# Performance work log

Hardware: AMD Instinct MI355X
Metric: run time of the kernel (lower is better)

Reference implementation:

```python
import jax, jax.numpy as jnp
import numpy as np

N = 50000   # nodes
E = 800000  # edges (avg degree 16)
D = 128     # node feature dim
DE = 16     # edge feature dim
H = 128     # MLP hidden dim
MSG_IN = 2 * D + DE + 1  # src feat + dst feat + edge feat + squared distance


def setup_inputs() -> dict:
    key = jax.random.key(0)
    ks = jax.random.split(key, 10)
    def wmat(k, shp):
        return jax.random.normal(k, shp, jnp.float32) * 0.05
    return {
        "f": jax.random.normal(ks[0], (N, D), jnp.float32),
        "x": jax.random.normal(ks[1], (N, 3), jnp.float32),
        "w": jax.random.normal(ks[2], (E, DE), jnp.float32),
        "src": jax.random.randint(ks[3], (E,), 0, N),
        "dst": jax.random.randint(ks[4], (E,), 0, N),
        "Wm1": wmat(ks[5], (MSG_IN, H)), "bm1": jnp.zeros((H,), jnp.float32),
        "Wm2": wmat(ks[6], (H, D)),      "bm2": jnp.zeros((D,), jnp.float32),
        "Wu1": wmat(ks[7], (D, H)),      "bu1": jnp.zeros((H,), jnp.float32),
        "Wu2": wmat(ks[8], (H, D)),      "bu2": jnp.zeros((D,), jnp.float32),
    }


def reference(f, x, w, src, dst, Wm1, bm1, Wm2, bm2, Wu1, bu1, Wu2, bu2):
    # message: gather endpoint features, squared distance, concat, MLP  [E, D]
    sqd = jnp.sum((x[src] - x[dst]) ** 2, axis=-1, keepdims=True)  # [E, 1]
    msg_in = jnp.concatenate([f[src], f[dst], w, sqd], axis=-1)    # [E, MSG_IN]
    m = jnp.dot(jax.nn.relu(jnp.dot(msg_in, Wm1) + bm1), Wm2) + bm2  # [E, D]
    # reduce: sum messages at destination nodes (DGL fn.sum)
    m_sum = jax.ops.segment_sum(m, dst, num_segments=N)             # [N, D]
    # update: node MLP on m_sum + f
    h = m_sum + f
    f_new = jnp.dot(jax.nn.relu(jnp.dot(h, Wu1) + bu1), Wu2) + bu2  # [N, D]
    return f_new
```

## Files before the change

### kernel.cpp

```cpp
#include <hip/hip_runtime.h>
#include <hip/hip_fp8.h>

#define D 128
#define HD 128
#define DE 16
#define MSG_IN 273
#define EB 64
#define NT 256
#define KP1 288
#define NCH2 4
#define NB 32
#define HID_PAD 132
#define CH8 (4 * EB * 64)
#define LDS1 (4 * EB * 64 + EB * 32)
#define OB 8192
#define OC 24576

typedef __attribute__((ext_vector_type(8))) short short8v;
typedef __attribute__((ext_vector_type(4))) float f32x4;
typedef __attribute__((ext_vector_type(2))) float f32x2;
typedef unsigned short ushort_t;
typedef unsigned char uchar_t;

#define GLOAD_LDS16(gp, lp) \
    __builtin_amdgcn_global_load_lds((const __attribute__((address_space(1))) unsigned int*)(gp), \
                                     (__attribute__((address_space(3))) unsigned int*)(lp), 16, 0, 0)

__device__ __forceinline__ unsigned short f2bf(float v) {
    unsigned int u = __builtin_bit_cast(unsigned int, v);
    u += 0x7fffu + ((u >> 16) & 1u);
    return (unsigned short)(u >> 16);
}
__device__ __forceinline__ float bf2f(ushort_t u) {
    return __builtin_bit_cast(float, (unsigned int)u << 16);
}
__device__ __forceinline__ unsigned int cvt_pk_bf16(float lo, float hi) {
    unsigned int r;
    asm("v_cvt_pk_bf16_f32 %0, %1, %2" : "=v"(r) : "v"(lo), "v"(hi));
    return r;
}
__device__ __forceinline__ uchar_t f8e(float v) {
    __hip_fp8_e4m3 t(v);
    return (uchar_t)t.__x;
}
__device__ __forceinline__ float f8d(unsigned b) {
    unsigned t = ((b & 0x7fu) << 20) | ((b & 0x80u) << 24);
    return __builtin_bit_cast(float, t) * 0x1p120f;
}

__global__ void fused_pre_kernel(const float* __restrict__ Wm1, const float* __restrict__ Wm2,
                                 const float* __restrict__ Wu1, const float* __restrict__ Wu2,
                                 ushort_t* __restrict__ W1p, ushort_t* __restrict__ W2p,
                                 ushort_t* __restrict__ Wu1p, ushort_t* __restrict__ Wu2p,
                                 const int* __restrict__ dst, int* __restrict__ cnt,
                                 int E) {
    const int gid    = blockIdx.x * 256 + threadIdx.x;
    const int stride = gridDim.x * 256;
    const int rp1 = 128 * KP1;
    const int rp2 = rp1 + HD * D;
    const int rp_elems = rp2 + 2 * HD * D;
    for (int i = gid; i < rp_elems; i += stride) {
        if (i < rp1) {
            int n = i / KP1, k = i % KP1;
            W1p[i] = f2bf((k < MSG_IN) ? Wm1[(size_t)k * HD + n] : 0.f);
        } else if (i < rp2) {
            int i2 = i - rp1;
            int n = i2 / HD, k = i2 % HD;
            W2p[i2] = f2bf(Wm2[(size_t)k * D + n]);
        } else {
            int i2 = (i - rp2);
            const bool second = i2 >= HD * D;
            if (second) i2 -= HD * D;
            int n = i2 / HD, k = i2 % HD;
            if (second) Wu2p[i2] = f2bf(Wu2[(size_t)k * D + n]);
            else        Wu1p[i2] = f2bf(Wu1[(size_t)k * HD + n]);
        }
    }
    for (int i = gid; i < E; i += stride) atomicAdd(&cnt[dst[i]], 1);
}

__global__ __launch_bounds__(1024) void scan_kernel(const int* __restrict__ cnt,
                                                    int* __restrict__ roff,
                                                    int* __restrict__ cursor, int Nn) {
    __shared__ int wsum[16];
    const int t = threadIdx.x, l = t & 63, wid = t >> 6;
    int running = 0;
    for (int base = 0; base < Nn; base += 4096) {
        const int i0 = base + t * 4;
        int v0 = 0, v1 = 0, v2 = 0, v3 = 0;
        if (i0 + 3 < Nn) {
            int4 v = *(const int4*)(cnt + i0);
            v0 = v.x; v1 = v.y; v2 = v.z; v3 = v.w;
        } else {
            if (i0 + 0 < Nn) v0 = cnt[i0 + 0];
            if (i0 + 1 < Nn) v1 = cnt[i0 + 1];
            if (i0 + 2 < Nn) v2 = cnt[i0 + 2];
        }
        const int vsum = v0 + v1 + v2 + v3;
        int s = vsum;
        #pragma unroll
        for (int off = 1; off < 64; off <<= 1) {
            int u = __shfl_up(s, off, 64);
            if (l >= off) s += u;
        }
        if (l == 63) wsum[wid] = s;
        __syncthreads();
        if (wid == 0 && l < 16) {
            int xv = wsum[l];
            #pragma unroll
            for (int off = 1; off < 16; off <<= 1) {
                int u = __shfl_up(xv, off, 64);
                if (l >= off) xv += u;
            }
            wsum[l] = xv;
        }
        __syncthreads();
        const int prev  = (wid > 0) ? wsum[wid - 1] : 0;
        const int total = wsum[15];
        int ex = running + prev + (s - vsum);
        if (i0 + 0 < Nn) { roff[i0 + 0] = ex; cursor[i0 + 0] = ex; } ex += v0;
        if (i0 + 1 < Nn) { roff[i0 + 1] = ex; cursor[i0 + 1] = ex; } ex += v1;
        if (i0 + 2 < Nn) { roff[i0 + 2] = ex; cursor[i0 + 2] = ex; } ex += v2;
        if (i0 + 3 < Nn) { roff[i0 + 3] = ex; cursor[i0 + 3] = ex; }
        running += total;
        __syncthreads();
    }
}

__global__ __launch_bounds__(NT, 4) void mid_kernel(
    const int* __restrict__ dst, int* cursor,
    const int* __restrict__ roff, const int* __restrict__ cnt,
    int* __restrict__ perm, int* __restrict__ sdst,
    const float* __restrict__ w, ushort_t* __restrict__ wbf,
    float* __restrict__ mh,
    const float* __restrict__ f, const ushort_t* __restrict__ W1p,
    uchar_t* __restrict__ Af, ushort_t* __restrict__ Bf16,
    int E, int Nn, int SB)
{
    if ((int)blockIdx.x < SB) {
        const int gid    = blockIdx.x * 256 + threadIdx.x;
        const int stride = SB * 256;
        for (int i = gid; i < E; i += stride) {
            int d = dst[i];
            int s = atomicAdd(&cursor[d], 1);
            perm[s] = i;
            sdst[s] = d;
            const float* wp = w + (size_t)i * DE;
            ushort_t* op = wbf + (size_t)i * DE;
            #pragma unroll
            for (int q = 0; q < 2; ++q) {
                float4 v0 = *(const float4*)(wp + q * 8);
                float4 v1 = *(const float4*)(wp + q * 8 + 4);
                union { ushort_t us[8]; short8v v; } pk;
                pk.us[0] = f2bf(v0.x); pk.us[1] = f2bf(v0.y);
                pk.us[2] = f2bf(v0.z); pk.us[3] = f2bf(v0.w);
                pk.us[4] = f2bf(v1.x); pk.us[5] = f2bf(v1.y);
                pk.us[6] = f2bf(v1.z); pk.us[7] = f2bf(v1.w);
                *(short8v*)(op + q * 8) = pk.v;
            }
        }
        for (int n = gid; n < Nn; n += stride) {
            const int c = cnt[n];
            const int r = roff[n];
            const bool need0 = (c == 0) || (r / EB != (r + c - 1) / EB);
            if (need0) {
                float4 z = {0.f, 0.f, 0.f, 0.f};
                float* p = mh + (size_t)n * D;
                #pragma unroll
                for (int k = 0; k < 32; ++k) *(float4*)(p + k * 4) = z;
            }
        }
        return;
    }

    __shared__ __align__(16) ushort_t lds[2 * 64 * 64];

    const int t    = threadIdx.x;
    const int lane = t & 63;
    const int wv   = t >> 6;
    const int col  = lane & 15;
    const int g    = lane >> 4;
    const int n0   = ((int)blockIdx.x - SB) * 64;

    #pragma unroll
    for (int it = 0; it < 4; ++it) {
        const int gidx = it * 256 + t;
        const int row  = gidx >> 4;
        const int gr   = gidx & 15;
        const int pair = gr >> 3, s = gr & 7;
        const int sP   = s ^ (row & 7);
        const int gn   = min(n0 + row, Nn - 1);
        const size_t off = (size_t)gn * D + gr * 8;
        float4 v0 = *(const float4*)(f + off);
        float4 v1 = *(const float4*)(f + off + 4);
        union { ushort_t us[8]; short8v v; } pk;
        pk.us[0] = f2bf(v0.x); pk.us[1] = f2bf(v0.y);
        pk.us[2] = f2bf(v0.z); pk.us[3] = f2bf(v0.w);
        pk.us[4] = f2bf(v1.x); pk.us[5] = f2bf(v1.y);
        pk.us[6] = f2bf(v1.z); pk.us[7] = f2bf(v1.w);
        *(short8v*)&lds[(pair * 64 + row) * 64 + sP * 8] = pk.v;
    }
    __syncthreads();

    #pragma unroll
    for (int half = 0; half < 2; ++half) {
        f32x4 acc[4][2];
        #pragma unroll
        for (int rt = 0; rt < 4; ++rt) {
            acc[rt][0] = (f32x4){0.f, 0.f, 0.f, 0.f};
            acc[rt][1] = (f32x4){0.f, 0.f, 0.f, 0.f};
        }
        const int kbase = half * 128;
        #pragma unroll
        for (int c = 0; c < 4; ++c) {
            short8v b0 = *(const short8v*)&W1p[(size_t)(wv * 32 + col) * KP1 + kbase + c * 32 + g * 8];
            short8v b1 = *(const short8v*)&W1p[(size_t)(wv * 32 + 16 + col) * KP1 + kbase + c * 32 + g * 8];
            short8v a[4];
            #pragma unroll
            for (int rt = 0; rt < 4; ++rt) {
                const int row = rt * 16 + col;
                const int sP = (((c & 1) << 2) + g) ^ (row & 7);
                a[rt] = *(const short8v*)&lds[((c >> 1) * 64 + row) * 64 + sP * 8];
            }
            #pragma unroll
            for (int rt = 0; rt < 4; ++rt) {
                acc[rt][0] = __builtin_amdgcn_mfma_f32_16x16x32_bf16(a[rt], b0, acc[rt][0], 0, 0, 0);
                acc[rt][1] = __builtin_amdgcn_mfma_f32_16x16x32_bf16(a[rt], b1, acc[rt][1], 0, 0, 0);
            }
        }
        #pragma unroll
        for (int rt = 0; rt < 4; ++rt)
            #pragma unroll
            for (int r = 0; r < 4; ++r) {
                const int row = rt * 16 + g * 4 + r;
                const int gn = n0 + row;
                if (gn < Nn) {
                    const int cp = wv * 32 + col * 2;
                    if (half == 0) {
                        ushort_t pk = (ushort_t)f8e(acc[rt][0][r]) |
                                      ((ushort_t)f8e(acc[rt][1][r]) << 8);
                        *(ushort_t*)(Af + (size_t)gn * D + cp) = pk;
                    } else {
                        *(unsigned int*)(Bf16 + (size_t)gn * D + cp) =
                            cvt_pk_bf16(acc[rt][0][r], acc[rt][1][r]);
                    }
                }
            }
    }
}

__global__ __launch_bounds__(NT, 5) void edge_lin_kernel(
    const uchar_t* __restrict__ Af, const ushort_t* __restrict__ Bf16,
    const float* __restrict__ x, const ushort_t* __restrict__ wbf,
    const int* __restrict__ src,
    const int* __restrict__ perm, const int* __restrict__ sdst,
    const ushort_t* __restrict__ W1p, const float* __restrict__ bm1,
    float* __restrict__ mh, int E)
{
    __shared__ __align__(16) uchar_t lds8[28672];
    __shared__ int s_rid[EB];
    __shared__ int s_dgs[EB];

    const int t    = threadIdx.x;
    const int lane = t & 63;
    const int wv   = t >> 6;
    const int e0   = blockIdx.x * EB;
    const int nvalid = min(EB, E - e0);

    const int myd  = (e0 + lane < E) ? sdst[e0 + lane] : -1;
    const int prevd = (e0 > 0) ? sdst[e0 - 1] : -2;
    const int nextd = (e0 + EB < E) ? sdst[e0 + EB] : -2;

    const int dprev_l = __shfl_up(myd, 1, 64);
    const bool head = (lane == 0) || (myd != dprev_l);
    const unsigned long long mask = __ballot(head && (lane < nvalid));
    const unsigned long long le = (lane == 63) ? ~0ull : ((1ull << (lane + 1)) - 1ull);
    const int rid = (int)__popcll(mask & le) - 1;
    const int ndist = (int)__popcll(mask);
    s_rid[lane] = (rid < 0) ? 0 : rid;
    if (head && lane < nvalid) s_dgs[rid] = myd;

    {
        const int el8 = lane >> 3;
        const int s   = lane & 7;
        const int sl  = s ^ el8;
        const int slA = min(e0 + wv * 16 + el8,     E - 1);
        const int slB = min(e0 + wv * 16 + 8 + el8, E - 1);
        const int nsA = src[perm[slA]];
        const int nsB = src[perm[slB]];
        GLOAD_LDS16(Af + (size_t)nsA * D + sl * 16, &lds8[(wv * 16    ) * 128]);
        GLOAD_LDS16(Af + (size_t)nsB * D + sl * 16, &lds8[(wv * 16 + 8) * 128]);
    }
    {
        const int ntask = ndist * 16;
        for (int idx = t; idx < ntask; idx += NT) {
            const int rowr = idx >> 4;
            const int gr   = idx & 15;
            const int dg   = s_dgs[rowr];
            uint4 v = *(const uint4*)(Bf16 + (size_t)dg * D + gr * 8);
            const int phys = gr ^ (rowr & 15);
            *(uint4*)&lds8[OB + rowr * 256 + phys * 16] = v;
        }
    }
    {
        const int el = lane >> 2, q = lane & 3;
        const int qp = q ^ (el & 3);
        const int slot = e0 + wv * 16 + el;
        const bool ok = slot < E;
        const int sc = min(slot, E - 1);
        const int ge = perm[sc];
        union { ushort_t us[8]; short8v v; } pk;
        #pragma unroll
        for (int j = 0; j < 8; ++j) pk.us[j] = 0;
        if (ok) {
            if (q < 2) {
                pk.v = *(const short8v*)(wbf + (size_t)ge * DE + q * 8);
            } else if (q == 2) {
                const int ns = src[ge], nd = sdst[sc];
                float dx = x[ns*3+0] - x[nd*3+0];
                float dy = x[ns*3+1] - x[nd*3+1];
                float dz = x[ns*3+2] - x[nd*3+2];
                pk.us[0] = f2bf(dx*dx + dy*dy + dz*dz);
            }
        }
        *(short8v*)&lds8[OC + (wv * 16 + el) * 64 + qp * 16] = pk.v;
    }

    const int col = lane & 15;
    const int g   = lane >> 4;

    short8v bc0 = *(const short8v*)&W1p[(size_t)(wv * 32 + col) * KP1 + 256 + g * 8];
    short8v bc1 = *(const short8v*)&W1p[(size_t)(wv * 32 + 16 + col) * KP1 + 256 + g * 8];

    __syncthreads();

    f32x4 acc[4][2];
    {
        float bv0 = bm1[wv * 32 + col];
        float bv1 = bm1[wv * 32 + 16 + col];
        #pragma unroll
        for (int rt = 0; rt < 4; ++rt) {
            acc[rt][0] = (f32x4){bv0, bv0, bv0, bv0};
            acc[rt][1] = (f32x4){bv1, bv1, bv1, bv1};
        }
    }
    #pragma unroll
    for (int rt = 0; rt < 4; ++rt) {
        const int row = rt * 16 + col;
        const int sP8 = g ^ (row & 3);
        short8v a = *(const short8v*)&lds8[OC + row * 64 + sP8 * 16];
        acc[rt][0] = __builtin_amdgcn_mfma_f32_16x16x32_bf16(a, bc0, acc[rt][0], 0, 0, 0);
        acc[rt][1] = __builtin_amdgcn_mfma_f32_16x16x32_bf16(a, bc1, acc[rt][1], 0, 0, 0);
    }

    float h[4][2][4];
    const int cgA = 2 * wv + (col >> 3);
    const int coA = (col * 2) & 15;
    const int cbB = 4 * wv + (col >> 2);
    const int coB = (col & 3) * 4;
    #pragma unroll
    for (int rt = 0; rt < 4; ++rt) {
        #pragma unroll
        for (int r = 0; r < 4; ++r) {
            const int row = rt * 16 + g * 4 + r;
            const int rd  = s_rid[row];
            const int aadr = row * 128 + ((cgA ^ (row & 7)) << 4) + coA;
            const int badr = OB + rd * 256 + ((cbB ^ (rd & 15)) << 4) + coB;
            const ushort_t ap = *(const ushort_t*)&lds8[aadr];
            const unsigned bp = *(const unsigned*)&lds8[badr];
            f32x2 af = __builtin_amdgcn_cvt_pk_f32_fp8((int)ap, false);
            const float b0f = __builtin_bit_cast(float, bp << 16);
            const float b1f = __builtin_bit_cast(float, bp & 0xffff0000u);
            h[rt][0][r] = fmaxf(acc[rt][0][r] + af[0] + b0f, 0.f);
            h[rt][1][r] = fmaxf(acc[rt][1][r] + af[1] + b1f, 0.f);
        }
    }

    float qs[4][2];
    #pragma unroll
    for (int rt = 0; rt < 4; ++rt) {
        qs[rt][0] = (h[rt][0][0] + h[rt][0][1]) + (h[rt][0][2] + h[rt][0][3]);
        qs[rt][1] = (h[rt][1][0] + h[rt][1][1]) + (h[rt][1][2] + h[rt][1][3]);
    }
    unsigned long long rem = mask;
    while (rem) {
        const int beg = (int)__builtin_ctzll(rem);
        rem &= rem - 1;
        const int end = rem ? (int)__builtin_ctzll(rem) : nvalid;
        const int dg  = __shfl(myd, beg, 64);

        float s0 = 0.f, s1 = 0.f;
        #pragma unroll
        for (int rt = 0; rt < 4; ++rt) {
            const int qb = rt * 16 + g * 4;
            const int lo = max(qb, beg);
            const int hi = min(qb + 4, end);
            if (lo < hi) {
                if (lo == qb && hi == qb + 4) {
                    s0 += qs[rt][0]; s1 += qs[rt][1];
                } else {
                    #pragma unroll
                    for (int r = 0; r < 4; ++r) {
                        const int sl = qb + r;
                        if (sl >= beg && sl < end) {
                            s0 += h[rt][0][r]; s1 += h[rt][1][r];
                        }
                    }
                }
            }
        }
        s0 += __shfl_xor(s0, 16, 64); s0 += __shfl_xor(s0, 32, 64);
        s1 += __shfl_xor(s1, 16, 64); s1 += __shfl_xor(s1, 32, 64);
        if (g == 0) {
            const bool bnd = (beg == 0 && dg == prevd) || (end == nvalid && dg == nextd);
            float* p = mh + (size_t)dg * D + wv * 32 + col;
            if (bnd) { atomicAdd(p, s0); atomicAdd(p + 16, s1); }
            else     { p[0] = s0; p[16] = s1; }
        }
    }
}

__global__ __launch_bounds__(NT, 4) void node_fused_kernel(
    const float* __restrict__ f, const float* __restrict__ mh,
    const int* __restrict__ cnt,
    const ushort_t* __restrict__ W2p, const float* __restrict__ bm2,
    const ushort_t* __restrict__ Wu1p, const float* __restrict__ bu1,
    const ushort_t* __restrict__ Wu2p, const float* __restrict__ bu2,
    float* __restrict__ out, int Nn)
{
    __shared__ __align__(16) ushort_t lds[2 * 64 * 64];
    __shared__ int s_cnt[64];

    const int t    = threadIdx.x;
    const int lane = t & 63;
    const int wv   = t >> 6;
    const int col  = lane & 15;
    const int g    = lane >> 4;
    const int n0   = blockIdx.x * 64;

    if (t < 64) s_cnt[t] = (n0 + t < Nn) ? cnt[n0 + t] : 0;

    #pragma unroll
    for (int it = 0; it < 4; ++it) {
        const int gidx = it * 256 + t;
        const int row  = gidx >> 4;
        const int gr   = gidx & 15;
        const int pair = gr >> 3, s = gr & 7;
        const int sP   = s ^ (row & 7);
        const int gn   = n0 + row;
        union { ushort_t us[8]; short8v v; } pk;
        if (gn < Nn) {
            const size_t off = (size_t)gn * D + gr * 8;
            float4 m0 = *(const float4*)(mh + off);
            float4 m1 = *(const float4*)(mh + off + 4);
            pk.us[0] = f2bf(m0.x); pk.us[1] = f2bf(m0.y);
            pk.us[2] = f2bf(m0.z); pk.us[3] = f2bf(m0.w);
            pk.us[4] = f2bf(m1.x); pk.us[5] = f2bf(m1.y);
            pk.us[6] = f2bf(m1.z); pk.us[7] = f2bf(m1.w);
        } else {
            #pragma unroll
            for (int j = 0; j < 8; ++j) pk.us[j] = 0;
        }
        *(short8v*)&lds[(pair * 64 + row) * 64 + sP * 8] = pk.v;
    }
    __syncthreads();

    f32x4 acc[4][2];
    {
        const float bv0 = bm2[wv * 32 + col];
        const float bv1 = bm2[wv * 32 + 16 + col];
        #pragma unroll
        for (int rt = 0; rt < 4; ++rt)
            #pragma unroll
            for (int r = 0; r < 4; ++r) {
                const float cn = (float)s_cnt[rt * 16 + g * 4 + r];
                acc[rt][0][r] = cn * bv0;
                acc[rt][1][r] = cn * bv1;
            }
    }
    #pragma unroll
    for (int c = 0; c < 4; ++c) {
        short8v b0 = *(const short8v*)&W2p[(size_t)(wv * 32 + col) * HD + c * 32 + g * 8];
        short8v b1 = *(const short8v*)&W2p[(size_t)(wv * 32 + 16 + col) * HD + c * 32 + g * 8];
        short8v a[4];
        #pragma unroll
        for (int rt = 0; rt < 4; ++rt) {
            const int row = rt * 16 + col;
            const int sP = (((c & 1) << 2) + g) ^ (row & 7);
            a[rt] = *(const short8v*)&lds[((c >> 1) * 64 + row) * 64 + sP * 8];
        }
        #pragma unroll
        for (int rt = 0; rt < 4; ++rt) {
            acc[rt][0] = __builtin_amdgcn_mfma_f32_16x16x32_bf16(a[rt], b0, acc[rt][0], 0, 0, 0);
            acc[rt][1] = __builtin_amdgcn_mfma_f32_16x16x32_bf16(a[rt], b1, acc[rt][1], 0, 0, 0);
        }
    }
    __syncthreads();

    const int ph = wv >> 1;
    #pragma unroll
    for (int rt = 0; rt < 4; ++rt)
        #pragma unroll
        for (int r = 0; r < 4; ++r) {
            const int row = rt * 16 + g * 4 + r;
            const int gn = n0 + row;
            #pragma unroll
            for (int j = 0; j < 2; ++j) {
                const int ca = wv * 32 + j * 16 + col;
                float v = 0.f;
                if (gn < Nn) v = acc[rt][j][r] + f[(size_t)gn * D + ca];
                unsigned int pk2 = cvt_pk_bf16(v, v);
                const int sH = (((wv & 1) << 2) + j * 2 + (col >> 3)) ^ (row & 7);
                lds[(ph * 64 + row) * 64 + sH * 8 + (col & 7)] = (ushort_t)pk2;
            }
        }
    __syncthreads();

    const size_t wrow0 = (size_t)(wv * 32 + col) * HD;
    const size_t wrow1 = (size_t)(wv * 32 + 16 + col) * HD;
    f32x4 acc1[4][2];
    {
        float bv0 = bu1[wv * 32 + col];
        float bv1 = bu1[wv * 32 + 16 + col];
        #pragma unroll
        for (int rt = 0; rt < 4; ++rt) {
            acc1[rt][0] = (f32x4){bv0, bv0, bv0, bv0};
            acc1[rt][1] = (f32x4){bv1, bv1, bv1, bv1};
        }
    }
    #pragma unroll
    for (int c = 0; c < 4; ++c) {
        short8v b0 = *(const short8v*)&Wu1p[wrow0 + c * 32 + g * 8];
        short8v b1 = *(const short8v*)&Wu1p[wrow1 + c * 32 + g * 8];
        short8v a[4];
        #pragma unroll
        for (int rt = 0; rt < 4; ++rt) {
            const int row = rt * 16 + col;
            const int sP = (((c & 1) << 2) + g) ^ (row & 7);
            a[rt] = *(const short8v*)&lds[((c >> 1) * 64 + row) * 64 + sP * 8];
        }
        #pragma unroll
        for (int rt = 0; rt < 4; ++rt) {
            acc1[rt][0] = __builtin_amdgcn_mfma_f32_16x16x32_bf16(a[rt], b0, acc1[rt][0], 0, 0, 0);
            acc1[rt][1] = __builtin_amdgcn_mfma_f32_16x16x32_bf16(a[rt], b1, acc1[rt][1], 0, 0, 0);
        }
    }
    __syncthreads();

    #pragma unroll
    for (int rt = 0; rt < 4; ++rt)
        #pragma unroll
        for (int j = 0; j < 2; ++j)
            #pragma unroll
            for (int r = 0; r < 4; ++r) {
                const int row = rt * 16 + g * 4 + r;
                float v = fmaxf(acc1[rt][j][r], 0.f);
                unsigned int pk2 = cvt_pk_bf16(v, v);
                const int sH = (((wv & 1) << 2) + j * 2 + (col >> 3)) ^ (row & 7);
                lds[(ph * 64 + row) * 64 + sH * 8 + (col & 7)] = (ushort_t)pk2;
            }
    __syncthreads();

    f32x4 acc2[4][2];
    {
        float bv0 = bu2[wv * 32 + col];
        float bv1 = bu2[wv * 32 + 16 + col];
        #pragma unroll
        for (int rt = 0; rt < 4; ++rt) {
            acc2[rt][0] = (f32x4){bv0, bv0, bv0, bv0};
            acc2[rt][1] = (f32x4){bv1, bv1, bv1, bv1};
        }
    }
    #pragma unroll
    for (int c = 0; c < 4; ++c) {
        short8v b0 = *(const short8v*)&Wu2p[wrow0 + c * 32 + g * 8];
        short8v b1 = *(const short8v*)&Wu2p[wrow1 + c * 32 + g * 8];
        short8v a[4];
        #pragma unroll
        for (int rt = 0; rt < 4; ++rt) {
            const int row = rt * 16 + col;
            const int sP = (((c & 1) << 2) + g) ^ (row & 7);
            a[rt] = *(const short8v*)&lds[((c >> 1) * 64 + row) * 64 + sP * 8];
        }
        #pragma unroll
        for (int rt = 0; rt < 4; ++rt) {
            acc2[rt][0] = __builtin_amdgcn_mfma_f32_16x16x32_bf16(a[rt], b0, acc2[rt][0], 0, 0, 0);
            acc2[rt][1] = __builtin_amdgcn_mfma_f32_16x16x32_bf16(a[rt], b1, acc2[rt][1], 0, 0, 0);
        }
    }

    #pragma unroll
    for (int rt = 0; rt < 4; ++rt)
        #pragma unroll
        for (int r = 0; r < 4; ++r) {
            const int row = rt * 16 + g * 4 + r;
            const int gn = n0 + row;
            if (gn < Nn) {
                out[(size_t)gn * D + wv * 32 + col]      = acc2[rt][0][r];
                out[(size_t)gn * D + wv * 32 + 16 + col] = acc2[rt][1][r];
            }
        }
}


__global__ void repack_kernel(const float* __restrict__ Wm1, const float* __restrict__ Wm2,
                              ushort_t* __restrict__ W1p, ushort_t* __restrict__ W2p) {
    int idx = blockIdx.x * 256 + threadIdx.x;
    const int n1 = 128 * KP1;
    if (idx < n1) {
        int n = idx / KP1, k = idx % KP1;
        W1p[idx] = f2bf((k < MSG_IN) ? Wm1[(size_t)k * HD + n] : 0.f);
    } else {
        int i2 = idx - n1;
        if (i2 < HD * D) {
            int n = i2 / HD, k = i2 % HD;
            W2p[i2] = f2bf(Wm2[(size_t)k * D + n]);
        }
    }
}

__global__ void fconv_kernel(const float* __restrict__ f, ushort_t* __restrict__ fb, int n8) {
    int i = blockIdx.x * 256 + threadIdx.x;
    if (i < n8) {
        float4 v0 = *(const float4*)(f + (size_t)i * 8);
        float4 v1 = *(const float4*)(f + (size_t)i * 8 + 4);
        union { ushort_t us[8]; short8v v; } pk;
        pk.us[0] = f2bf(v0.x); pk.us[1] = f2bf(v0.y);
        pk.us[2] = f2bf(v0.z); pk.us[3] = f2bf(v0.w);
        pk.us[4] = f2bf(v1.x); pk.us[5] = f2bf(v1.y);
        pk.us[6] = f2bf(v1.z); pk.us[7] = f2bf(v1.w);
        *(short8v*)(fb + (size_t)i * 8) = pk.v;
    }
}

__global__ __launch_bounds__(NT, 4) void edge_mfma_kernel(
    const ushort_t* __restrict__ fbf, const float* __restrict__ x,
    const float* __restrict__ w, const int* __restrict__ src,
    const int* __restrict__ dst,
    const ushort_t* __restrict__ W1p, const float* __restrict__ bm1,
    const ushort_t* __restrict__ W2p, const float* __restrict__ bm2,
    ushort_t* msum, int E)
{
    __shared__ __align__(16) ushort_t lds[LDS1];
    __shared__ int s_dst[EB];

    const int t    = threadIdx.x;
    const int lane = t & 63;
    const int wv   = t >> 6;
    const int e0   = blockIdx.x * EB;

    if (t < EB) s_dst[t] = (e0 + t < E) ? dst[e0 + t] : 0;
    {
        const int el8 = lane >> 3;
        const int s   = lane & 7;
        const int sl  = s ^ el8;
        const int geA = min(e0 + wv * 16 + el8,     E - 1);
        const int geB = min(e0 + wv * 16 + 8 + el8, E - 1);
        const int nsA = src[geA], ndA = dst[geA];
        const int nsB = src[geB], ndB = dst[geB];
        #pragma unroll
        for (int p = 0; p < 4; ++p) {
            const int n0 = (p < 2) ? nsA : ndA;
            const int n1 = (p < 2) ? nsB : ndB;
            const ushort_t* g0 = fbf + (size_t)n0 * D + (p & 1) * 64 + sl * 8;
            const ushort_t* g1 = fbf + (size_t)n1 * D + (p & 1) * 64 + sl * 8;
            GLOAD_LDS16(g0, &lds[(p * EB + wv * 16    ) * 64]);
            GLOAD_LDS16(g1, &lds[(p * EB + wv * 16 + 8) * 64]);
        }
    }
    {
        const int el = lane >> 2, q = lane & 3;
        const int qp = q ^ (el & 3);
        const int ge = e0 + wv * 16 + el;
        const bool ok = ge < E;
        const int gc = min(ge, E - 1);
        union { ushort_t us[8]; short8v v; } pk;
        #pragma unroll
        for (int j = 0; j < 8; ++j) pk.us[j] = 0;
        if (ok) {
            if (q < 2) {
                float4 w0 = *(const float4*)(w + (size_t)gc * DE + q * 8);
                float4 w1 = *(const float4*)(w + (size_t)gc * DE + q * 8 + 4);
                pk.us[0] = f2bf(w0.x); pk.us[1] = f2bf(w0.y);
                pk.us[2] = f2bf(w0.z); pk.us[3] = f2bf(w0.w);
                pk.us[4] = f2bf(w1.x); pk.us[5] = f2bf(w1.y);
                pk.us[6] = f2bf(w1.z); pk.us[7] = f2bf(w1.w);
            } else if (q == 2) {
                const int ns = src[gc], nd = dst[gc];
                float dx = x[ns*3+0] - x[nd*3+0];
                float dy = x[ns*3+1] - x[nd*3+1];
                float dz = x[ns*3+2] - x[nd*3+2];
                pk.us[0] = f2bf(dx*dx + dy*dy + dz*dz);
            }
        }
        *(short8v*)&lds[CH8 + (wv * 16 + el) * 32 + qp * 8] = pk.v;
    }

    const int col = lane & 15;
    const int g   = lane >> 4;
    const size_t wrow0 = (size_t)(wv * 32 + col) * KP1;
    const size_t wrow1 = (size_t)(wv * 32 + 16 + col) * KP1;
    short8v nb0 = *(const short8v*)&W1p[wrow0 + g * 8];
    short8v nb1 = *(const short8v*)&W1p[wrow1 + g * 8];
    __syncthreads();

    f32x4 acc[4][2];
    {
        float bv0 = bm1[wv * 32 + col];
        float bv1 = bm1[wv * 32 + 16 + col];
        #pragma unroll
        for (int rt = 0; rt < 4; ++rt) {
            acc[rt][0] = (f32x4){bv0, bv0, bv0, bv0};
            acc[rt][1] = (f32x4){bv1, bv1, bv1, bv1};
        }
    }
    #pragma unroll
    for (int c = 0; c < 9; ++c) {
        short8v b0 = nb0, b1 = nb1;
        if (c + 1 < 9) {
            nb0 = *(const short8v*)&W1p[wrow0 + (c + 1) * 32 + g * 8];
            nb1 = *(const short8v*)&W1p[wrow1 + (c + 1) * 32 + g * 8];
        }
        short8v a[4];
        #pragma unroll
        for (int rt = 0; rt < 4; ++rt) {
            const int row = rt * 16 + col;
            if (c < 8) {
                const int sP = (((c & 1) << 2) + g) ^ (row & 7);
                a[rt] = *(const short8v*)&lds[((c >> 1) * EB + row) * 64 + sP * 8];
            } else {
                const int sP = g ^ (row & 3);
                a[rt] = *(const short8v*)&lds[CH8 + row * 32 + sP * 8];
            }
        }
        #pragma unroll
        for (int rt = 0; rt < 4; ++rt) {
            acc[rt][0] = __builtin_amdgcn_mfma_f32_16x16x32_bf16(a[rt], b0, acc[rt][0], 0, 0, 0);
            acc[rt][1] = __builtin_amdgcn_mfma_f32_16x16x32_bf16(a[rt], b1, acc[rt][1], 0, 0, 0);
        }
    }
    __syncthreads();

    const int ph = wv >> 1;
    #pragma unroll
    for (int rt = 0; rt < 4; ++rt)
        #pragma unroll
        for (int j = 0; j < 2; ++j)
            #pragma unroll
            for (int r = 0; r < 4; ++r) {
                const int row = rt * 16 + g * 4 + r;
                float v = fmaxf(acc[rt][j][r], 0.f);
                unsigned int pk2 = cvt_pk_bf16(v, v);
                const int sH = (((wv & 1) << 2) + j * 2 + (col >> 3)) ^ (row & 7);
                lds[(ph * EB + row) * 64 + sH * 8 + (col & 7)] = (ushort_t)pk2;
            }
    __syncthreads();

    const size_t w2r0 = (size_t)(wv * 32 + col) * HD;
    const size_t w2r1 = (size_t)(wv * 32 + 16 + col) * HD;
    short8v m0 = *(const short8v*)&W2p[w2r0 + g * 8];
    short8v m1 = *(const short8v*)&W2p[w2r1 + g * 8];
    f32x4 acc2[4][2];
    {
        float bv0 = bm2[wv * 32 + col];
        float bv1 = bm2[wv * 32 + 16 + col];
        #pragma unroll
        for (int rt = 0; rt < 4; ++rt) {
            acc2[rt][0] = (f32x4){bv0, bv0, bv0, bv0};
            acc2[rt][1] = (f32x4){bv1, bv1, bv1, bv1};
        }
    }
    #pragma unroll
    for (int c = 0; c < NCH2; ++c) {
        short8v b0 = m0, b1 = m1;
        if (c + 1 < NCH2) {
            m0 = *(const short8v*)&W2p[w2r0 + (c + 1) * 32 + g * 8];
            m1 = *(const short8v*)&W2p[w2r1 + (c + 1) * 32 + g * 8];
        }
        short8v a[4];
        #pragma unroll
        for (int rt = 0; rt < 4; ++rt) {
            const int row = rt * 16 + col;
            const int sP = (((c & 1) << 2) + g) ^ (row & 7);
            a[rt] = *(const short8v*)&lds[((c >> 1) * EB + row) * 64 + sP * 8];
        }
        #pragma unroll
        for (int rt = 0; rt < 4; ++rt) {
            acc2[rt][0] = __builtin_amdgcn_mfma_f32_16x16x32_bf16(a[rt], b0, acc2[rt][0], 0, 0, 0);
            acc2[rt][1] = __builtin_amdgcn_mfma_f32_16x16x32_bf16(a[rt], b1, acc2[rt][1], 0, 0, 0);
        }
    }

    const bool even = (col & 1) == 0;
    #pragma unroll
    for (int rt = 0; rt < 4; ++rt)
        #pragma unroll
        for (int r = 0; r < 4; ++r) {
            const int e  = rt * 16 + g * 4 + r;
            const int ge = e0 + e;
            const int dg = s_dst[e];
            #pragma unroll
            for (int j = 0; j < 2; ++j) {
                float v  = acc2[rt][j][r];
                float vn = __shfl_xor(v, 1, 64);
                if (even && ge < E) {
                    unsigned int pk2 = cvt_pk_bf16(v, vn);
                    ushort_t* p = msum + (size_t)dg * D + wv * 32 + j * 16 + col;
                    asm volatile("global_atomic_pk_add_bf16 %0, %1, off"
                                 :: "v"(p), "v"(pk2) : "memory");
                }
            }
        }
}

template<bool MB16>
__global__ __launch_bounds__(NT, 4) void node_kernel(
    const float* __restrict__ f, const void* __restrict__ msum_v,
    const float* __restrict__ Wu1, const float* __restrict__ bu1,
    const float* __restrict__ Wu2, const float* __restrict__ bu2,
    float* out, int Nn)
{
    __shared__ __align__(16) float hin[NB][HID_PAD];
    __shared__ __align__(16) float hid[NB][HID_PAD];
    const int t  = threadIdx.x;
    const int n0 = blockIdx.x * NB;
    const int nn = min(NB, Nn - n0);

    {
        #pragma unroll
        for (int it = 0; it < 4; ++it) {
            const int idx = it * 1024 + t * 4;
            const int e   = idx >> 7;
            const int cb  = idx & 127;
            if (e < nn) {
                const size_t off = (size_t)(n0 + e) * D + cb;
                float4 mv;
                if (MB16) {
                    uint2 pk = *(const uint2*)((const ushort_t*)msum_v + off);
                    mv.x = bf2f((ushort_t)(pk.x & 0xffffu));
                    mv.y = bf2f((ushort_t)(pk.x >> 16));
                    mv.z = bf2f((ushort_t)(pk.y & 0xffffu));
                    mv.w = bf2f((ushort_t)(pk.y >> 16));
                } else {
                    mv = *(const float4*)((const float*)msum_v + off);
                }
                float4 fv = *(const float4*)&f[off];
                float4 o = {mv.x + fv.x, mv.y + fv.y, mv.z + fv.z, mv.w + fv.w};
                *(float4*)&hin[e][cb] = o;
            }
        }
    }
    __syncthreads();

    const int tc = t & 15, te2 = (t >> 4) * 2, c0 = tc * 8;
    float a1[2][8];
    #pragma unroll
    for (int c = 0; c < 8; ++c) { float bv = bu1[c0 + c]; a1[0][c] = bv; a1[1][c] = bv; }
    for (int i = 0; i < D; i += 4) {
        float m0[4], m1[4];
        *(float4*)m0 = *(const float4*)&hin[te2][i];
        *(float4*)m1 = *(const float4*)&hin[te2 + 1][i];
        #pragma unroll
        for (int r = 0; r < 4; ++r) {
            float wr[8];
            *(float4*)&wr[0] = *(const float4*)(Wu1 + (size_t)(i + r) * HD + c0);
            *(float4*)&wr[4] = *(const float4*)(Wu1 + (size_t)(i + r) * HD + c0 + 4);
            #pragma unroll
            for (int c = 0; c < 8; ++c) { a1[0][c] += m0[r]*wr[c]; a1[1][c] += m1[r]*wr[c]; }
        }
    }
    #pragma unroll
    for (int j = 0; j < 2; ++j) {
        float v[8];
        #pragma unroll
        for (int c = 0; c < 8; ++c) v[c] = fmaxf(a1[j][c], 0.f);
        *(float4*)&hid[te2 + j][c0] = *(float4*)&v[0];
        *(float4*)&hid[te2 + j][c0 + 4] = *(float4*)&v[4];
    }
    __syncthreads();
    float a2[2][8];
    #pragma unroll
    for (int c = 0; c < 8; ++c) { float bv = bu2[c0 + c]; a2[0][c] = bv; a2[1][c] = bv; }
    for (int h = 0; h < HD; h += 4) {
        float m0[4], m1[4];
        *(float4*)m0 = *(const float4*)&hid[te2][h];
        *(float4*)m1 = *(const float4*)&hid[te2 + 1][h];
        #pragma unroll
        for (int r = 0; r < 4; ++r) {
            float wr[8];
            *(float4*)&wr[0] = *(const float4*)(Wu2 + (size_t)(h + r) * D + c0);
            *(float4*)&wr[4] = *(const float4*)(Wu2 + (size_t)(h + r) * D + c0 + 4);
            #pragma unroll
            for (int c = 0; c < 8; ++c) { a2[0][c] += m0[r]*wr[c]; a2[1][c] += m1[r]*wr[c]; }
        }
    }
    #pragma unroll
    for (int j = 0; j < 2; ++j) {
        int e = te2 + j, gn = n0 + e;
        if (e < nn) {
            *(float4*)(out + (size_t)gn * D + c0) = *(float4*)&a2[j][0];
            *(float4*)(out + (size_t)gn * D + c0 + 4) = *(float4*)&a2[j][4];
        }
    }
}

extern "C" void kernel_launch(void* const* d_in, const int* in_sizes, int n_in,
                              void* d_out, int out_size, void* d_ws, size_t ws_size,
                              hipStream_t stream) {
    const float* f   = (const float*)d_in[0];
    const float* x   = (const float*)d_in[1];
    const float* w   = (const float*)d_in[2];
    const int*   src = (const int*)d_in[3];
    const int*   dst = (const int*)d_in[4];
    const float* Wm1 = (const float*)d_in[5];
    const float* bm1 = (const float*)d_in[6];
    const float* Wm2 = (const float*)d_in[7];
    const float* bm2 = (const float*)d_in[8];
    const float* Wu1 = (const float*)d_in[9];
    const float* bu1 = (const float*)d_in[10];
    const float* Wu2 = (const float*)d_in[11];
    const float* bu2 = (const float*)d_in[12];

    const int Nn = in_sizes[0] / D;
    const int E  = in_sizes[3];

    const size_t wbytes  = (size_t)(128 * KP1 + HD * D) * sizeof(ushort_t);
    const size_t wubytes = (size_t)(2 * HD * D) * sizeof(ushort_t);
    auto align512 = [](size_t v) { return (v + 511) & ~(size_t)511; };
    char* wsb = (char*)d_ws;

    size_t off = 0;
    const size_t o_w    = off; off = align512(off + wbytes);
    const size_t o_wu   = off; off = align512(off + wubytes);
    const size_t o_wbf  = off; off = align512(off + (size_t)E * DE * 2);
    const size_t o_af   = off; off = align512(off + (size_t)Nn * D);
    const size_t o_bf16 = off; off = align512(off + (size_t)Nn * D * 2);
    const size_t o_cnt  = off; off = align512(off + (size_t)Nn * 4);
    const size_t o_roff = off; off = align512(off + (size_t)Nn * 4);
    const size_t o_cur  = off; off = align512(off + (size_t)Nn * 4);
    const size_t o_perm = off; off = align512(off + (size_t)E * 4);
    const size_t o_sdst = off; off = align512(off + (size_t)E * 4);
    const size_t o_mh   = off; off = align512(off + (size_t)Nn * D * 4);
    const size_t primary_total = off;

    if (ws_size >= primary_total) {
        ushort_t* W1p  = (ushort_t*)(wsb + o_w);
        ushort_t* W2p  = W1p + 128 * KP1;
        ushort_t* Wu1p = (ushort_t*)(wsb + o_wu);
        ushort_t* Wu2p = Wu1p + HD * D;
        ushort_t* wbf  = (ushort_t*)(wsb + o_wbf);
        uchar_t*  Af   = (uchar_t*)(wsb + o_af);
        ushort_t* Bf16 = (ushort_t*)(wsb + o_bf16);
        int* cnt       = (int*)(wsb + o_cnt);
        int* roff      = (int*)(wsb + o_roff);
        int* cursor    = (int*)(wsb + o_cur);
        int* perm      = (int*)(wsb + o_perm);
        int* sdst      = (int*)(wsb + o_sdst);
        float* mh      = (float*)(wsb + o_mh);

        const int ntiles = (E + EB - 1) / EB;
        const int nblk   = (Nn + 63) / 64;
        const int SB     = (E + 511) / 512;
        hipMemsetAsync(cnt, 0, (size_t)Nn * 4, stream);
        fused_pre_kernel<<<dim3(1024), dim3(256), 0, stream>>>(
            Wm1, Wm2, Wu1, Wu2, W1p, W2p, Wu1p, Wu2p, dst, cnt, E);
        scan_kernel<<<dim3(1), dim3(1024), 0, stream>>>(cnt, roff, cursor, Nn);
        mid_kernel<<<dim3(SB + nblk), dim3(NT), 0, stream>>>(
            dst, cursor, roff, cnt, perm, sdst, w, wbf, mh,
            f, W1p, Af, Bf16, E, Nn, SB);
        edge_lin_kernel<<<dim3(ntiles), dim3(NT), 0, stream>>>(
            Af, Bf16, x, wbf, src, perm, sdst, W1p, bm1, mh, E);
        node_fused_kernel<<<dim3(nblk), dim3(NT), 0, stream>>>(
            f, mh, cnt, W2p, bm2, Wu1p, bu1, Wu2p, bu2, (float*)d_out, Nn);
        return;
    }

    size_t off2 = 0;
    const size_t p_w  = off2; off2 = align512(off2 + wbytes);
    const size_t p_fb = off2; off2 = align512(off2 + (size_t)Nn * D * 2);
    const size_t p_ms = off2; off2 = align512(off2 + (size_t)Nn * D * 2);
    if (ws_size >= off2) {
        ushort_t* W1p  = (ushort_t*)(wsb + p_w);
        ushort_t* W2p  = W1p + 128 * KP1;
        ushort_t* fbf  = (ushort_t*)(wsb + p_fb);
        ushort_t* msum = (ushort_t*)(wsb + p_ms);
        const int rp_elems = 128 * KP1 + HD * D;
        hipMemsetAsync(msum, 0, (size_t)Nn * D * 2, stream);
        repack_kernel<<<dim3((rp_elems + 255) / 256), dim3(256), 0, stream>>>(Wm1, Wm2, W1p, W2p);
        const int n8 = Nn * D / 8;
        fconv_kernel<<<dim3((n8 + 255) / 256), dim3(256), 0, stream>>>(f, fbf, n8);
        edge_mfma_kernel<<<dim3((E + EB - 1) / EB), dim3(NT), 0, stream>>>(
            fbf, x, w, src, dst, W1p, bm1, W2p, bm2, msum, E);
        node_kernel<true><<<dim3((Nn + NB - 1) / NB), dim3(NT), 0, stream>>>(
            f, msum, Wu1, bu1, Wu2, bu2, (float*)d_out, Nn);
        return;
    }
}
```

Measured before the change: 239.4 us.

## Cap LDS-staged dst rows in edge kernel and move weight repack into mid_kernel

The edge kernel now stages at most BCAP distinct destination rows of Bf16 in LDS and reads any further rows straight from global memory. This cuts LDS from 28 KB to 20 KB so the launch bound can rise from 5 to 7 blocks per CU. Separately, the Wm2/Wu1/Wu2 bf16 repack moves from the pre kernel into 24 extra blocks of mid_kernel, which shortens the serial pre kernel. The cost is uncached global loads for tiles with many distinct destinations and possible register pressure under the tighter launch bound.

Result: slower. 300.7 us (+25.6%).

```diff
diff --git a/kernel.cpp b/kernel.cpp
--- a/kernel.cpp
+++ b/kernel.cpp
@@ -14,7 +14,8 @@
 #define CH8 (4 * EB * 64)
 #define LDS1 (4 * EB * 64 + EB * 32)
 #define OB 8192
-#define OC 24576
+#define OC 16384
+#define BCAP 32
 
 typedef __attribute__((ext_vector_type(8))) short short8v;
 typedef __attribute__((ext_vector_type(4))) float f32x4;
@@ -48,33 +49,16 @@
     return __builtin_bit_cast(float, t) * 0x1p120f;
 }
 
-__global__ void fused_pre_kernel(const float* __restrict__ Wm1, const float* __restrict__ Wm2,
-                                 const float* __restrict__ Wu1, const float* __restrict__ Wu2,
-                                 ushort_t* __restrict__ W1p, ushort_t* __restrict__ W2p,
-                                 ushort_t* __restrict__ Wu1p, ushort_t* __restrict__ Wu2p,
+__global__ void fused_pre_kernel(const float* __restrict__ Wm1,
+                                 ushort_t* __restrict__ W1p,
                                  const int* __restrict__ dst, int* __restrict__ cnt,
                                  int E) {
     const int gid    = blockIdx.x * 256 + threadIdx.x;
     const int stride = gridDim.x * 256;
     const int rp1 = 128 * KP1;
-    const int rp2 = rp1 + HD * D;
-    const int rp_elems = rp2 + 2 * HD * D;
-    for (int i = gid; i < rp_elems; i += stride) {
-        if (i < rp1) {
-            int n = i / KP1, k = i % KP1;
-            W1p[i] = f2bf((k < MSG_IN) ? Wm1[(size_t)k * HD + n] : 0.f);
-        } else if (i < rp2) {
-            int i2 = i - rp1;
-            int n = i2 / HD, k = i2 % HD;
-            W2p[i2] = f2bf(Wm2[(size_t)k * D + n]);
-        } else {
-            int i2 = (i - rp2);
-            const bool second = i2 >= HD * D;
-            if (second) i2 -= HD * D;
-            int n = i2 / HD, k = i2 % HD;
-            if (second) Wu2p[i2] = f2bf(Wu2[(size_t)k * D + n]);
-            else        Wu1p[i2] = f2bf(Wu1[(size_t)k * HD + n]);
-        }
+    for (int i = gid; i < rp1; i += stride) {
+        int n = i / KP1, k = i % KP1;
+        W1p[i] = f2bf((k < MSG_IN) ? Wm1[(size_t)k * HD + n] : 0.f);
     }
     for (int i = gid; i < E; i += stride) atomicAdd(&cnt[dst[i]], 1);
 }
@@ -135,10 +119,13 @@
     float* __restrict__ mh,
     const float* __restrict__ f, const ushort_t* __restrict__ W1p,
     uchar_t* __restrict__ Af, ushort_t* __restrict__ Bf16,
-    int E, int Nn, int SB)
+    const float* __restrict__ Wm2, const float* __restrict__ Wu1, const float* __restrict__ Wu2,
+    ushort_t* __restrict__ W2p, ushort_t* __restrict__ Wu1p, ushort_t* __restrict__ Wu2p,
+    int E, int Nn, int SB, int AB)
 {
-    if ((int)blockIdx.x < SB) {
-        const int gid    = blockIdx.x * 256 + threadIdx.x;
+    const int bid = (int)blockIdx.x;
+    if (bid < SB) {
+        const int gid    = bid * 256 + threadIdx.x;
         const int stride = SB * 256;
         for (int i = gid; i < E; i += stride) {
             int d = dst[i];
@@ -172,6 +159,27 @@
         }
         return;
     }
+    if (bid >= SB + AB) {
+        const int rb0   = SB + AB;
+        const int gid    = (bid - rb0) * 256 + threadIdx.x;
+        const int stride = ((int)gridDim.x - rb0) * 256;
+        const int r1 = HD * D;
+        const int total = 3 * HD * D;
+        for (int i = gid; i < total; i += stride) {
+            if (i < r1) {
+                int n = i / HD, k = i % HD;
+                W2p[i] = f2bf(Wm2[(size_t)k * D + n]);
+            } else {
+                int i2 = i - r1;
+                const bool second = i2 >= HD * D;
+                if (second) i2 -= HD * D;
+                int n = i2 / HD, k = i2 % HD;
+                if (second) Wu2p[i2] = f2bf(Wu2[(size_t)k * D + n]);
+                else        Wu1p[i2] = f2bf(Wu1[(size_t)k * HD + n]);
+            }
+        }
+        return;
+    }
 
     __shared__ __align__(16) ushort_t lds[2 * 64 * 64];
 
@@ -180,7 +188,7 @@
     const int wv   = t >> 6;
     const int col  = lane & 15;
     const int g    = lane >> 4;
-    const int n0   = ((int)blockIdx.x - SB) * 64;
+    const int n0   = (bid - SB) * 64;
 
     #pragma unroll
     for (int it = 0; it < 4; ++it) {
@@ -249,7 +257,7 @@
     }
 }
 
-__global__ __launch_bounds__(NT, 5) void edge_lin_kernel(
+__global__ __launch_bounds__(NT, 7) void edge_lin_kernel(
     const uchar_t* __restrict__ Af, const ushort_t* __restrict__ Bf16,
     const float* __restrict__ x, const ushort_t* __restrict__ wbf,
     const int* __restrict__ src,
@@ -257,7 +265,7 @@
     const ushort_t* __restrict__ W1p, const float* __restrict__ bm1,
     float* __restrict__ mh, int E)
 {
-    __shared__ __align__(16) uchar_t lds8[28672];
+    __shared__ __align__(16) uchar_t lds8[20480];
     __shared__ int s_rid[EB];
     __shared__ int s_dgs[EB];
 
@@ -292,7 +300,8 @@
         GLOAD_LDS16(Af + (size_t)nsB * D + sl * 16, &lds8[(wv * 16 + 8) * 128]);
     }
     {
-        const int ntask = ndist * 16;
+        const int ncap  = min(ndist, BCAP);
+        const int ntask = ncap * 16;
         for (int idx = t; idx < ntask; idx += NT) {
             const int rowr = idx >> 4;
             const int gr   = idx & 15;
@@ -365,9 +374,16 @@
             const int row = rt * 16 + g * 4 + r;
             const int rd  = s_rid[row];
             const int aadr = row * 128 + ((cgA ^ (row & 7)) << 4) + coA;
-            const int badr = OB + rd * 256 + ((cbB ^ (rd & 15)) << 4) + coB;
             const ushort_t ap = *(const ushort_t*)&lds8[aadr];
-            const unsigned bp = *(const unsigned*)&lds8[badr];
+            unsigned bp;
+            if (rd < BCAP) {
+                const int badr = OB + rd * 256 + ((cbB ^ (rd & 15)) << 4) + coB;
+                bp = *(const unsigned*)&lds8[badr];
+            } else {
+                const int dg2 = s_dgs[rd];
+                bp = *(const unsigned*)((const uchar_t*)Bf16 +
+                        (size_t)dg2 * 256 + (size_t)wv * 64 + col * 4);
+            }
             f32x2 af = __builtin_amdgcn_cvt_pk_f32_fp8((int)ap, false);
             const float b0f = __builtin_bit_cast(float, bp << 16);
             const float b1f = __builtin_bit_cast(float, bp & 0xffff0000u);
@@ -961,13 +977,15 @@
         const int ntiles = (E + EB - 1) / EB;
         const int nblk   = (Nn + 63) / 64;
         const int SB     = (E + 511) / 512;
+        const int RB     = 24;
         hipMemsetAsync(cnt, 0, (size_t)Nn * 4, stream);
         fused_pre_kernel<<<dim3(1024), dim3(256), 0, stream>>>(
-            Wm1, Wm2, Wu1, Wu2, W1p, W2p, Wu1p, Wu2p, dst, cnt, E);
+            Wm1, W1p, dst, cnt, E);
         scan_kernel<<<dim3(1), dim3(1024), 0, stream>>>(cnt, roff, cursor, Nn);
-        mid_kernel<<<dim3(SB + nblk), dim3(NT), 0, stream>>>(
+        mid_kernel<<<dim3(SB + nblk + RB), dim3(NT), 0, stream>>>(
             dst, cursor, roff, cnt, perm, sdst, w, wbf, mh,
-            f, W1p, Af, Bf16, E, Nn, SB);
+            f, W1p, Af, Bf16, Wm2, Wu1, Wu2, W2p, Wu1p, Wu2p,
+            E, Nn, SB, nblk);
         edge_lin_kernel<<<dim3(ntiles), dim3(NT), 0, stream>>>(
             Af, Bf16, x, wbf, src, perm, sdst, W1p, bm1, mh, E);
         node_fused_kernel<<<dim3(nblk), dim3(NT), 0, stream>>>(
```
